# Optimization experiments

Measured on AMD Instinct MI355X. Metric: run time of the kernel, lower is better.

The kernel has to match this reference:

```python
import jax, jax.numpy as jnp
import numpy as np

N = 128  # padded Hadamard size (find_min_power(122))
H1 = W1 = 122

def _hadamard(n):
    H = np.array([[1.0]], dtype=np.float32)
    while H.shape[0] < n:
        H = np.block([[H, H], [H, -H]])
    return H

_H = jnp.asarray(_hadamard(N))  # symmetric 128x128 +/-1 matrix
_DN = ('NCHW', 'OIHW', 'NCHW')

def _conv(x, w, b, stride, pad):
    y = jax.lax.conv_general_dilated(x, w, (stride, stride),
                                     [(pad, pad), (pad, pad)], dimension_numbers=_DN)
    return y + b[None, :, None, None]

def _convT(x, w, b, stride, pad):
    # torch ConvTranspose2d weight layout [in, out, kh, kw]
    k = w.shape[-1]
    wf = jnp.flip(w, (2, 3)).transpose(1, 0, 2, 3)  # -> [out, in, kh, kw]
    p = k - 1 - pad
    y = jax.lax.conv_general_dilated(x, wf, (1, 1), [(p, p), (p, p)],
                                     lhs_dilation=(stride, stride), dimension_numbers=_DN)
    return y + b[None, :, None, None]

def _fwht2(x):
    # fwht along -1 then -2 (dense Hadamard matmul, matching fast=False path)
    x = jnp.einsum('bchw,wk->bchk', x, _H)
    return jnp.einsum('bchw,hk->bckw', x, _H)

def _ifwht2(x):
    x = jnp.einsum('bchw,wk->bchk', x, _H) / N
    return jnp.einsum('bchw,hk->bckw', x, _H) / N

def _pad(x):
    return jnp.pad(x, ((0, 0), (0, 0), (0, N - H1), (0, N - W1)))

def _thresh(x, T):
    aT = jnp.abs(T)
    s = jnp.copysign(jax.nn.relu(jnp.abs(x) - aT), x)
    return s + jnp.sign(s) * aT

def _kl(q):
    e = q.size // 64
    p = jax.nn.sigmoid(jnp.full((64,), 0.001, q.dtype))
    qm = jnp.sum(jax.nn.sigmoid(jnp.abs(q).reshape(e, 64)), axis=0) / e
    return jnp.sum(p * jnp.log(p / qm)) + jnp.sum((1 - p) * jnp.log((1 - p) / (1 - qm)))

def _tv(x, weight):
    b, c, h, w = x.shape
    tv = jnp.abs(x[:, :, 1:, :] - x[:, :, :-1, :]).sum() + \
         jnp.abs(x[:, :, :, 1:] - x[:, :, :, :-1]).sum()
    return weight * tv / (b * c * h * w)

def setup_inputs() -> dict:
    key = jax.random.key(0)
    ks = jax.random.split(key, 16)
    B = 128
    inp = {
        'x': jax.random.normal(ks[0], (B, 1, 256, 256), jnp.float32),
        'val': 0,
        'v1': jax.random.uniform(ks[1], (N, N), jnp.float32),
        'T1': jax.random.uniform(ks[2], (N, N), jnp.float32) / 10,
        'v2': jax.random.uniform(ks[3], (N, N), jnp.float32),
        'T2': jax.random.uniform(ks[4], (N, N), jnp.float32) / 10,
        'v3': jax.random.uniform(ks[5], (N, N), jnp.float32),
        'T3': jax.random.uniform(ks[6], (N, N), jnp.float32) / 10,
        'w1': jax.random.normal(ks[7], (4, 1, 16, 16), jnp.float32) * 0.05,
        'b1': jax.random.normal(ks[8], (4,), jnp.float32) * 0.01,
        'w2': jax.random.normal(ks[9], (4, 4, 7, 7), jnp.float32) * 0.05,
        'b2': jax.random.normal(ks[10], (4,), jnp.float32) * 0.01,
        'w3': jax.random.normal(ks[11], (4, 4, 7, 7), jnp.float32) * 0.05,  # [in,out,kh,kw]
        'b3': jax.random.normal(ks[12], (4,), jnp.float32) * 0.01,
        'w4': jax.random.normal(ks[13], (4, 1, 16, 16), jnp.float32) * 0.05,  # [in,out,kh,kw]
        'b4': jax.random.normal(ks[14], (1,), jnp.float32) * 0.01,
    }
    return inp

def reference(x, val, v1, T1, v2, T2, v3, T3, w1, b1, w2, b2, w3, b3, w4, b4):
    TV_WEIGHT = 0.05  # original draws np.random.uniform(0, 0.1); fixed for determinism
    x1 = _conv(x, w1, b1, 2, 1)                       # [B,4,122,122]
    x6 = _thresh(v1 * _fwht2(_pad(x1)), T1)           # [B,4,128,128]
    x9 = _ifwht2(x6)[..., :H1, :W1]
    x10 = _conv(x9, w2, b2, 1, 3)                     # [B,4,122,122]
    x15 = _thresh(v2 * _fwht2(_pad(x10)), T2)
    x18 = _ifwht2(x15)[..., :H1, :W1]
    x19 = _convT(x18, w3, b3, 1, 3) + x10
    x24 = _thresh(v3 * _fwht2(_pad(x19)), T3)
    x27 = _ifwht2(x24 + x6)[..., :H1, :W1]
    out = _convT(x27, w4, b4, 2, 1) * x               # [B,1,256,256]
    loss = 1.0 * _tv(out, TV_WEIGHT) + 0.1 * (_kl(x6) + _kl(x15) + _kl(x24))
    return out, loss
```

## Files before the change

### kernel.cpp

```cpp
#include <hip/hip_runtime.h>
#include <math.h>

#define PLANE 16384
#define NPLANES 512

__device__ __forceinline__ void fwht2d_reg(float* __restrict__ v, float* __restrict__ xch,
                                           int W, int L) {
#pragma unroll
    for (int m = 1; m <= 2; m <<= 1) {
#pragma unroll
        for (int r = 0; r < 64; ++r) {
            if (!(r & m)) {
                int s = r | m;
                float a = v[r], b = v[s];
                v[r] = a + b; v[s] = a - b;
            }
        }
    }
#pragma unroll
    for (int m = 1; m <= 32; m <<= 1) {
        float sg = (L & m) ? -1.f : 1.f;
#pragma unroll
        for (int r = 0; r < 64; ++r) {
            float p = __shfl_xor(v[r], m);
            v[r] = fmaf(sg, v[r], p);
        }
    }
#pragma unroll
    for (int m = 4; m <= 32; m <<= 1) {
#pragma unroll
        for (int r = 0; r < 64; ++r) {
            if (!(r & m)) {
                int s = r | m;
                float a = v[r], b = v[s];
                v[r] = a + b; v[s] = a - b;
            }
        }
    }
#pragma unroll
    for (int mw = 1; mw <= 2; mw <<= 1) {
        int Wp = W ^ mw;
        float sg = (W & mw) ? -1.f : 1.f;
#pragma unroll
        for (int half = 0; half < 2; ++half) {
            __syncthreads();
#pragma unroll
            for (int j = 0; j < 32; ++j)
                xch[(j * 4 + W) * 64 + L] = v[half * 32 + j];
            __syncthreads();
#pragma unroll
            for (int j = 0; j < 32; ++j) {
                float p = xch[(j * 4 + Wp) * 64 + L];
                v[half * 32 + j] = fmaf(sg, v[half * 32 + j], p);
            }
        }
    }
}

template <bool STORET, bool ADD>
__global__ __launch_bounds__(256) void fwht_kernel_t(
    const float* __restrict__ in, const float* __restrict__ vmat,
    const float* __restrict__ tmat, const float* __restrict__ addbuf,
    float* __restrict__ outThresh, float* __restrict__ outInv,
    float* __restrict__ klpart)
{
    __shared__ float xch[32 * 256];
    const int tid = threadIdx.x;
    const int W = tid >> 6, L = tid & 63;
    const int plane = blockIdx.x;
    const int hbase = W * 32 + ((L >> 5) << 4);
    const int wbase = (L & 31) << 2;
    const float* src = in + (size_t)plane * PLANE;

    float v[64];
#pragma unroll
    for (int g = 0; g < 16; ++g) {
        float4 t = *(const float4*)&src[(hbase + g) * 128 + wbase];
        v[4 * g] = t.x; v[4 * g + 1] = t.y; v[4 * g + 2] = t.z; v[4 * g + 3] = t.w;
    }

    fwht2d_reg(v, xch, W, L);

    float ls0 = 0.f, ls1 = 0.f, ls2 = 0.f, ls3 = 0.f;
#pragma unroll
    for (int g = 0; g < 16; ++g) {
        int rowoff = (hbase + g) * 128 + wbase;
        float4 vm = *(const float4*)&vmat[rowoff];
        float4 tm = *(const float4*)&tmat[rowoff];
        float y0 = v[4 * g]     * vm.x;
        float y1 = v[4 * g + 1] * vm.y;
        float y2 = v[4 * g + 2] * vm.z;
        float y3 = v[4 * g + 3] * vm.w;
        y0 = (fabsf(y0) > fabsf(tm.x)) ? y0 : 0.f;
        y1 = (fabsf(y1) > fabsf(tm.y)) ? y1 : 0.f;
        y2 = (fabsf(y2) > fabsf(tm.z)) ? y2 : 0.f;
        y3 = (fabsf(y3) > fabsf(tm.w)) ? y3 : 0.f;
        ls0 += 1.f / (1.f + __expf(-fabsf(y0)));
        ls1 += 1.f / (1.f + __expf(-fabsf(y1)));
        ls2 += 1.f / (1.f + __expf(-fabsf(y2)));
        ls3 += 1.f / (1.f + __expf(-fabsf(y3)));
        if (STORET) {
            float4 o; o.x = y0; o.y = y1; o.z = y2; o.w = y3;
            *(float4*)&outThresh[(size_t)plane * PLANE + rowoff] = o;
        }
        if (ADD) {
            float4 ad = *(const float4*)&addbuf[(size_t)plane * PLANE + rowoff];
            y0 += ad.x; y1 += ad.y; y2 += ad.z; y3 += ad.w;
        }
        v[4 * g] = y0; v[4 * g + 1] = y1; v[4 * g + 2] = y2; v[4 * g + 3] = y3;
    }
#pragma unroll
    for (int m = 16; m <= 32; m <<= 1) {
        ls0 += __shfl_xor(ls0, m);
        ls1 += __shfl_xor(ls1, m);
        ls2 += __shfl_xor(ls2, m);
        ls3 += __shfl_xor(ls3, m);
    }
    if (L < 16) {
        float4 o; o.x = ls0; o.y = ls1; o.z = ls2; o.w = ls3;
        *(float4*)&klpart[(size_t)(plane * 4 + W) * 64 + 4 * L] = o;
    }

    fwht2d_reg(v, xch, W, L);

    float* dst = outInv + (size_t)plane * PLANE;
    const float s = 1.f / 16384.f;
#pragma unroll
    for (int g = 0; g < 16; ++g) {
        int h = hbase + g;
        bool rv = h < 122;
        float4 o;
        o.x = (rv && wbase + 0 < 122) ? v[4 * g]     * s : 0.f;
        o.y = (rv && wbase + 1 < 122) ? v[4 * g + 1] * s : 0.f;
        o.z = (rv && wbase + 2 < 122) ? v[4 * g + 2] * s : 0.f;
        o.w = (rv && wbase + 3 < 122) ? v[4 * g + 3] * s : 0.f;
        *(float4*)&dst[h * 128 + wbase] = o;
    }
}

__global__ void prep_weights(const float* __restrict__ w3, const float* __restrict__ w4,
                             float* __restrict__ w3c, float* __restrict__ w4p)
{
    int tid = blockIdx.x * 256 + threadIdx.x;
    if (tid < 784) {
        int oc = tid / 196;
        int rem = tid - oc * 196;
        int ic = rem / 49;
        int k = rem - ic * 49;
        int kh = k / 7, kw = k - kh * 7;
        w3c[(oc * 4 + ic) * 49 + k] = w3[(ic * 4 + oc) * 49 + (6 - kh) * 7 + (6 - kw)];
    }
    if (tid < 1024) {
        int u = tid & 7, t = (tid >> 3) & 7, pb = (tid >> 6) & 1, pa = (tid >> 7) & 1, ic = tid >> 8;
        int kh = 2 * t + (pa ? 0 : 1);
        int kw = 2 * u + (pb ? 0 : 1);
        w4p[tid] = w4[ic * 256 + kh * 16 + kw];
    }
}

__global__ __launch_bounds__(256) void conv1_kernel(
    const float* __restrict__ x, const float* __restrict__ w1,
    const float* __restrict__ b1, float* __restrict__ out)
{
    __shared__ float tile[78][80];
    int tx = blockIdx.x, ty = blockIdx.y, b = blockIdx.z;
    int tid = threadIdx.x;
    const float* xp = x + (size_t)b * 65536;
    int r0g = ty * 64 - 1, c0g = tx * 64 - 1;
    for (int i = tid; i < 78 * 78; i += 256) {
        int rr = i / 78, cc = i - rr * 78;
        int gi = r0g + rr, gj = c0g + cc;
        tile[rr][cc] = (gi >= 0 && gi < 256 && gj >= 0 && gj < 256) ? xp[gi * 256 + gj] : 0.f;
    }
    __syncthreads();
    int cg = tid & 7, r = tid >> 3;
    int B = cg * 4;
    float acc[4][4];
#pragma unroll
    for (int oc = 0; oc < 4; ++oc)
#pragma unroll
        for (int c = 0; c < 4; ++c) acc[oc][c] = 0.f;
#pragma unroll 1
    for (int kh = 0; kh < 16; ++kh) {
        float win[24];
        const float* trow = &tile[2 * r + kh][2 * B];
#pragma unroll
        for (int k = 0; k < 6; ++k)
            *(float4*)&win[4 * k] = *(const float4*)&trow[4 * k];
#pragma unroll
        for (int oc = 0; oc < 4; ++oc) {
            const float* wr = w1 + oc * 256 + kh * 16;
#pragma unroll
            for (int kw = 0; kw < 16; ++kw) {
                float wv = wr[kw];
#pragma unroll
                for (int c = 0; c < 4; ++c)
                    acc[oc][c] = fmaf(win[2 * c + kw], wv, acc[oc][c]);
            }
        }
    }
    int oh = ty * 32 + r;
    int owb = tx * 32 + B;
    bool rowv = oh < 122;
#pragma unroll
    for (int oc = 0; oc < 4; ++oc) {
        float bv = b1[oc];
        float4 res;
        res.x = (rowv && owb + 0 < 122) ? acc[oc][0] + bv : 0.f;
        res.y = (rowv && owb + 1 < 122) ? acc[oc][1] + bv : 0.f;
        res.z = (rowv && owb + 2 < 122) ? acc[oc][2] + bv : 0.f;
        res.w = (rowv && owb + 3 < 122) ? acc[oc][3] + bv : 0.f;
        *(float4*)&out[(((size_t)b * 4 + oc) << 14) + (oh << 7) + owb] = res;
    }
}

__global__ __launch_bounds__(256) void conv7_kernel(
    const float* __restrict__ in, const float* __restrict__ w,
    const float* __restrict__ bias, const float* __restrict__ skip,
    float* __restrict__ out)
{
    __shared__ float tile[4][38][40];
    int tx = blockIdx.x, ty = blockIdx.y, b = blockIdx.z;
    int tid = threadIdx.x;
    int r0g = ty * 32 - 3, c0g = tx * 32 - 3;
    for (int i = tid; i < 4 * 38 * 38; i += 256) {
        int ic = i / 1444;
        int rem = i - ic * 1444;
        int rr = rem / 38, cc = rem - rr * 38;
        int gi = r0g + rr, gj = c0g + cc;
        float v = 0.f;
        if (gi >= 0 && gi < 128 && gj >= 0 && gj < 128)
            v = in[(((size_t)b * 4 + ic) << 14) + (gi << 7) + gj];
        tile[ic][rr][cc] = v;
    }
    __syncthreads();
    int cg = tid & 7, r = tid >> 3;
    int B = cg * 4;
    float acc[4][4];
#pragma unroll
    for (int oc = 0; oc < 4; ++oc)
#pragma unroll
        for (int c = 0; c < 4; ++c) acc[oc][c] = 0.f;
#pragma unroll 1
    for (int ic = 0; ic < 4; ++ic) {
#pragma unroll 1
        for (int kh = 0; kh < 7; ++kh) {
            float win[12];
            const float* trow = &tile[ic][r + kh][B];
#pragma unroll
            for (int k = 0; k < 3; ++k)
                *(float4*)&win[4 * k] = *(const float4*)&trow[4 * k];
#pragma unroll
            for (int oc = 0; oc < 4; ++oc) {
                const float* wr = w + (oc * 4 + ic) * 49 + kh * 7;
#pragma unroll
                for (int kw = 0; kw < 7; ++kw) {
                    float wv = wr[kw];
#pragma unroll
                    for (int c = 0; c < 4; ++c)
                        acc[oc][c] = fmaf(win[c + kw], wv, acc[oc][c]);
                }
            }
        }
    }
    int oh = ty * 32 + r;
    int owb = tx * 32 + B;
    bool rowv = oh < 122;
#pragma unroll
    for (int oc = 0; oc < 4; ++oc) {
        size_t o = (((size_t)b * 4 + oc) << 14) + (oh << 7) + owb;
        float4 sv = make_float4(0.f, 0.f, 0.f, 0.f);
        if (skip) sv = *(const float4*)&skip[o];
        float bv = bias[oc];
        float4 res;
        res.x = (rowv && owb + 0 < 122) ? acc[oc][0] + bv + sv.x : 0.f;
        res.y = (rowv && owb + 1 < 122) ? acc[oc][1] + bv + sv.y : 0.f;
        res.z = (rowv && owb + 2 < 122) ? acc[oc][2] + bv + sv.z : 0.f;
        res.w = (rowv && owb + 3 < 122) ? acc[oc][3] + bv + sv.w : 0.f;
        *(float4*)&out[o] = res;
    }
}

#define CT_HALF(T, ROW, PA)                                                    \
    _Pragma("unroll")                                                          \
    for (int pb = 0; pb < 2; ++pb) {                                           \
        const float* w8 = wp + (((ic * 2 + (PA)) * 2 + pb) * 8 + (T)) * 8;     \
        _Pragma("unroll")                                                      \
        for (int u = 0; u < 8; ++u) {                                          \
            float wv = w8[u];                                                  \
            _Pragma("unroll")                                                  \
            for (int c = 0; c < 4; ++c)                                        \
                acc[PA][pb][c] = fmaf(ROW[8 + c + pb - u], wv, acc[PA][pb][c]);\
        }                                                                      \
    }

__global__ __launch_bounds__(256) void convt4_kernel(
    const float* __restrict__ in, const float* __restrict__ wp,
    const float* __restrict__ bias, const float* __restrict__ xin,
    float* __restrict__ out)
{
    __shared__ float tile[4][40][44];
    int tx = blockIdx.x, ty = blockIdx.y, b = blockIdx.z;
    int tid = threadIdx.x;
    int A0 = ty * 32, B0 = tx * 32;
    int r0g = A0 - 7, c0g = B0 - 8;
    for (int i = tid; i < 4 * 40 * 44; i += 256) {
        int ic = i / 1760;
        int rem = i - ic * 1760;
        int rr = rem / 44, cc = rem - rr * 44;
        int gi = r0g + rr, gj = c0g + cc;
        float v = 0.f;
        if (gi >= 0 && gi < 128 && gj >= 0 && gj < 128)
            v = in[(((size_t)b * 4 + ic) << 14) + (gi << 7) + gj];
        tile[ic][rr][cc] = v;
    }
    __syncthreads();
    int cg = tid & 7, ra = tid >> 3;
    float acc[2][2][4];
#pragma unroll
    for (int pa = 0; pa < 2; ++pa)
#pragma unroll
        for (int pb = 0; pb < 2; ++pb)
#pragma unroll
            for (int c = 0; c < 4; ++c) acc[pa][pb][c] = 0.f;
#pragma unroll 1
    for (int ic = 0; ic < 4; ++ic) {
        float bufA[16], bufB[16];
#pragma unroll
        for (int k = 0; k < 4; ++k)
            *(float4*)&bufB[4 * k] = *(const float4*)&tile[ic][ra + 8][4 * cg + 4 * k];
#pragma unroll 1
        for (int t2 = 0; t2 < 8; t2 += 2) {
#pragma unroll
            for (int k = 0; k < 4; ++k)
                *(float4*)&bufA[4 * k] = *(const float4*)&tile[ic][ra + 7 - t2][4 * cg + 4 * k];
            CT_HALF(t2, bufA, 0)
            CT_HALF(t2, bufB, 1)
#pragma unroll
            for (int k = 0; k < 4; ++k)
                *(float4*)&bufB[4 * k] = *(const float4*)&tile[ic][ra + 6 - t2][4 * cg + 4 * k];
            CT_HALF(t2 + 1, bufB, 0)
            CT_HALF(t2 + 1, bufA, 1)
        }
    }
    int oh0 = 2 * (A0 + ra);
    int owb = 2 * (B0 + 4 * cg);
    float bv = bias[0];
#pragma unroll
    for (int pa = 0; pa < 2; ++pa) {
        size_t o = (size_t)b * 65536 + (size_t)(oh0 + pa) * 256 + owb;
        float4 x0 = *(const float4*)&xin[o];
        float4 x1 = *(const float4*)&xin[o + 4];
        float4 r0, r1;
        r0.x = (acc[pa][0][0] + bv) * x0.x;
        r0.y = (acc[pa][1][0] + bv) * x0.y;
        r0.z = (acc[pa][0][1] + bv) * x0.z;
        r0.w = (acc[pa][1][1] + bv) * x0.w;
        r1.x = (acc[pa][0][2] + bv) * x1.x;
        r1.y = (acc[pa][1][2] + bv) * x1.y;
        r1.z = (acc[pa][0][3] + bv) * x1.z;
        r1.w = (acc[pa][1][3] + bv) * x1.w;
        *(float4*)&out[o] = r0;
        *(float4*)&out[o + 4] = r1;
    }
}

__global__ __launch_bounds__(256) void tv_kernel(
    const float* __restrict__ out, float* __restrict__ tvpart)
{
    __shared__ float red[256];
    int tid = threadIdx.x;
    float local = 0.f;
    const int total = 128 * 65536;
    for (int idx = blockIdx.x * 256 + tid; idx < total; idx += gridDim.x * 256) {
        float v = out[idx];
        int hw = idx & 65535;
        if (hw < 65280) local += fabsf(out[idx + 256] - v);
        if ((idx & 255) != 255) local += fabsf(out[idx + 1] - v);
    }
    red[tid] = local;
    __syncthreads();
    for (int s = 128; s > 0; s >>= 1) {
        if (tid < s) red[tid] += red[tid + s];
        __syncthreads();
    }
    if (tid == 0) tvpart[blockIdx.x] = red[0];
}

__global__ __launch_bounds__(256) void reduce1_kernel(
    const float* __restrict__ klpart, const float* __restrict__ tvpart,
    float* __restrict__ klred, float* __restrict__ tvred)
{
    int bid = blockIdx.x;
    int tid = threadIdx.x;
    if (bid < 48) {
        int layer = bid >> 4, chunk = bid & 15;
        int sub = tid >> 6, t = tid & 63;
        const float* base = klpart + (size_t)layer * 131072 + (size_t)chunk * 128 * 64;
        float s = 0.f;
        for (int r = sub; r < 128; r += 4)
            s += base[r * 64 + t];
        __shared__ float red[4][64];
        red[sub][t] = s;
        __syncthreads();
        if (tid < 64)
            klred[(layer * 16 + chunk) * 64 + tid] =
                red[0][tid] + red[1][tid] + red[2][tid] + red[3][tid];
    } else {
        __shared__ float red[256];
        float s = 0.f;
        for (int i = tid; i < 2048; i += 256) s += tvpart[i];
        red[tid] = s;
        __syncthreads();
        for (int st = 128; st > 0; st >>= 1) {
            if (tid < st) red[tid] += red[tid + st];
            __syncthreads();
        }
        if (tid == 0) tvred[0] = red[0];
    }
}

__global__ __launch_bounds__(64) void finalize2_kernel(
    const float* __restrict__ klred, const float* __restrict__ tvred,
    float* __restrict__ lossout)
{
    int t = threadIdx.x;
    float p = 1.f / (1.f + __expf(-0.001f));
    float term = 0.f;
#pragma unroll
    for (int l = 0; l < 3; ++l) {
        float q = 0.f;
#pragma unroll
        for (int c = 0; c < 16; ++c)
            q += klred[(l * 16 + c) * 64 + t];
        float qm = q * (1.f / 131072.f);
        term += p * logf(p / qm) + (1.f - p) * logf((1.f - p) / (1.f - qm));
    }
#pragma unroll
    for (int off = 32; off > 0; off >>= 1)
        term += __shfl_down(term, off);
    if (t == 0)
        lossout[0] = 0.05f * tvred[0] / 8388608.f + 0.1f * term;
}

extern "C" void kernel_launch(void* const* d_in, const int* in_sizes, int n_in,
                              void* d_out, int out_size, void* d_ws, size_t ws_size,
                              hipStream_t stream) {
    (void)in_sizes; (void)n_in; (void)out_size; (void)ws_size;
    const float* x  = (const float*)d_in[0];
    const float* v1 = (const float*)d_in[2];
    const float* T1 = (const float*)d_in[3];
    const float* v2 = (const float*)d_in[4];
    const float* T2 = (const float*)d_in[5];
    const float* v3 = (const float*)d_in[6];
    const float* T3 = (const float*)d_in[7];
    const float* w1 = (const float*)d_in[8];
    const float* b1 = (const float*)d_in[9];
    const float* w2 = (const float*)d_in[10];
    const float* b2 = (const float*)d_in[11];
    const float* w3 = (const float*)d_in[12];
    const float* b3 = (const float*)d_in[13];
    const float* w4 = (const float*)d_in[14];
    const float* b4 = (const float*)d_in[15];
    float* out = (float*)d_out;

    float* W0 = (float*)d_ws;
    float* W1 = W0 + (size_t)NPLANES * PLANE;
    float* W2 = W1 + (size_t)NPLANES * PLANE;
    float* klpart = W2 + (size_t)NPLANES * PLANE;
    float* tvpart = klpart + 3 * 2048 * 64;
    float* klred  = tvpart + 2048;
    float* tvred  = klred + 3072;
    float* w3c = tvred + 64;
    float* w4p = w3c + 784;
    float* x10buf = out;

    prep_weights<<<4, 256, 0, stream>>>(w3, w4, w3c, w4p);
    conv1_kernel<<<dim3(4, 4, 128), 256, 0, stream>>>(x, w1, b1, W0);
    fwht_kernel_t<true, false><<<NPLANES, 256, 0, stream>>>(W0, v1, T1, nullptr, W1, W2, klpart);
    conv7_kernel<<<dim3(4, 4, 128), 256, 0, stream>>>(W2, w2, b2, nullptr, x10buf);
    fwht_kernel_t<false, false><<<NPLANES, 256, 0, stream>>>(x10buf, v2, T2, nullptr, nullptr, W0, klpart + 131072);
    conv7_kernel<<<dim3(4, 4, 128), 256, 0, stream>>>(W0, w3c, b3, x10buf, W2);
    fwht_kernel_t<false, true><<<NPLANES, 256, 0, stream>>>(W2, v3, T3, W1, nullptr, W0, klpart + 2 * 131072);
    convt4_kernel<<<dim3(4, 4, 128), 256, 0, stream>>>(W0, w4p, b4, x, out);
    tv_kernel<<<2048, 256, 0, stream>>>(out, tvpart);
    reduce1_kernel<<<49, 256, 0, stream>>>(klpart, tvpart, klred, tvred);
    finalize2_kernel<<<1, 64, 0, stream>>>(klred, tvred, out + 8388608);
}
```

Before: 375.0 us.

## Register-block two input rows per thread in convT and vectorize TV loss

```diff
diff --git a/kernel.cpp b/kernel.cpp
--- a/kernel.cpp
+++ b/kernel.cpp
@@ -281,7 +281,7 @@
     }
 }
 
-#define CT_HALF(T, ROW, PA)                                                    \
+#define APPLY(P, T, ROW, PA)                                                   \
     _Pragma("unroll")                                                          \
     for (int pb = 0; pb < 2; ++pb) {                                           \
         const float* w8 = wp + (((ic * 2 + (PA)) * 2 + pb) * 8 + (T)) * 8;     \
@@ -290,93 +290,116 @@
             float wv = w8[u];                                                  \
             _Pragma("unroll")                                                  \
             for (int c = 0; c < 4; ++c)                                        \
-                acc[PA][pb][c] = fmaf(ROW[8 + c + pb - u], wv, acc[PA][pb][c]);\
+                acc[P][PA][pb][c] = fmaf(ROW[8 + c + pb - u], wv, acc[P][PA][pb][c]); \
         }                                                                      \
     }
+
+#define LOADROW(BUF, R)                                                        \
+    _Pragma("unroll")                                                          \
+    for (int k = 0; k < 4; ++k)                                                \
+        *(float4*)&BUF[4 * k] = *(const float4*)&tld[(R) * 44 + 4 * cg + 4 * k];
 
 __global__ __launch_bounds__(256) void convt4_kernel(
     const float* __restrict__ in, const float* __restrict__ wp,
     const float* __restrict__ bias, const float* __restrict__ xin,
     float* __restrict__ out)
 {
-    __shared__ float tile[4][40][44];
+    __shared__ float tile[4][72][44];
     int tx = blockIdx.x, ty = blockIdx.y, b = blockIdx.z;
     int tid = threadIdx.x;
-    int A0 = ty * 32, B0 = tx * 32;
+    int A0 = ty * 64, B0 = tx * 32;
     int r0g = A0 - 7, c0g = B0 - 8;
-    for (int i = tid; i < 4 * 40 * 44; i += 256) {
-        int ic = i / 1760;
-        int rem = i - ic * 1760;
+    float* tl = &tile[0][0][0];
+    for (int i = tid; i < 4 * 72 * 44; i += 256) {
+        int ic = i / 3168;
+        int rem = i - ic * 3168;
         int rr = rem / 44, cc = rem - rr * 44;
         int gi = r0g + rr, gj = c0g + cc;
         float v = 0.f;
         if (gi >= 0 && gi < 128 && gj >= 0 && gj < 128)
             v = in[(((size_t)b * 4 + ic) << 14) + (gi << 7) + gj];
-        tile[ic][rr][cc] = v;
+        tl[i] = v;
     }
     __syncthreads();
-    int cg = tid & 7, ra = tid >> 3;
-    float acc[2][2][4];
-#pragma unroll
-    for (int pa = 0; pa < 2; ++pa)
-#pragma unroll
-        for (int pb = 0; pb < 2; ++pb)
-#pragma unroll
-            for (int c = 0; c < 4; ++c) acc[pa][pb][c] = 0.f;
+    int cg = tid & 7, tr = tid >> 3;
+    int rb = 2 * tr;
+    float acc[2][2][2][4];
+#pragma unroll
+    for (int p = 0; p < 2; ++p)
+#pragma unroll
+        for (int pa = 0; pa < 2; ++pa)
+#pragma unroll
+            for (int pb = 0; pb < 2; ++pb)
+#pragma unroll
+                for (int c = 0; c < 4; ++c) acc[p][pa][pb][c] = 0.f;
 #pragma unroll 1
     for (int ic = 0; ic < 4; ++ic) {
-        float bufA[16], bufB[16];
-#pragma unroll
-        for (int k = 0; k < 4; ++k)
-            *(float4*)&bufB[4 * k] = *(const float4*)&tile[ic][ra + 8][4 * cg + 4 * k];
-#pragma unroll 1
-        for (int t2 = 0; t2 < 8; t2 += 2) {
-#pragma unroll
-            for (int k = 0; k < 4; ++k)
-                *(float4*)&bufA[4 * k] = *(const float4*)&tile[ic][ra + 7 - t2][4 * cg + 4 * k];
-            CT_HALF(t2, bufA, 0)
-            CT_HALF(t2, bufB, 1)
-#pragma unroll
-            for (int k = 0; k < 4; ++k)
-                *(float4*)&bufB[4 * k] = *(const float4*)&tile[ic][ra + 6 - t2][4 * cg + 4 * k];
-            CT_HALF(t2 + 1, bufB, 0)
-            CT_HALF(t2 + 1, bufA, 1)
-        }
-    }
-    int oh0 = 2 * (A0 + ra);
+        const float* tld = &tile[ic][0][0];
+        float rA[16], rB[16];
+        LOADROW(rA, rb + 9)
+        LOADROW(rB, rb + 8)
+        APPLY(1, 0, rA, 1)
+        LOADROW(rA, rb + 7)
+        APPLY(0, 0, rB, 1) APPLY(1, 0, rB, 0) APPLY(1, 1, rB, 1)
+        LOADROW(rB, rb + 6)
+        APPLY(0, 0, rA, 0) APPLY(0, 1, rA, 1) APPLY(1, 1, rA, 0) APPLY(1, 2, rA, 1)
+        LOADROW(rA, rb + 5)
+        APPLY(0, 1, rB, 0) APPLY(0, 2, rB, 1) APPLY(1, 2, rB, 0) APPLY(1, 3, rB, 1)
+        LOADROW(rB, rb + 4)
+        APPLY(0, 2, rA, 0) APPLY(0, 3, rA, 1) APPLY(1, 3, rA, 0) APPLY(1, 4, rA, 1)
+        LOADROW(rA, rb + 3)
+        APPLY(0, 3, rB, 0) APPLY(0, 4, rB, 1) APPLY(1, 4, rB, 0) APPLY(1, 5, rB, 1)
+        LOADROW(rB, rb + 2)
+        APPLY(0, 4, rA, 0) APPLY(0, 5, rA, 1) APPLY(1, 5, rA, 0) APPLY(1, 6, rA, 1)
+        LOADROW(rA, rb + 1)
+        APPLY(0, 5, rB, 0) APPLY(0, 6, rB, 1) APPLY(1, 6, rB, 0) APPLY(1, 7, rB, 1)
+        LOADROW(rB, rb + 0)
+        APPLY(0, 6, rA, 0) APPLY(0, 7, rA, 1) APPLY(1, 7, rA, 0)
+        APPLY(0, 7, rB, 0)
+    }
     int owb = 2 * (B0 + 4 * cg);
     float bv = bias[0];
 #pragma unroll
-    for (int pa = 0; pa < 2; ++pa) {
-        size_t o = (size_t)b * 65536 + (size_t)(oh0 + pa) * 256 + owb;
-        float4 x0 = *(const float4*)&xin[o];
-        float4 x1 = *(const float4*)&xin[o + 4];
-        float4 r0, r1;
-        r0.x = (acc[pa][0][0] + bv) * x0.x;
-        r0.y = (acc[pa][1][0] + bv) * x0.y;
-        r0.z = (acc[pa][0][1] + bv) * x0.z;
-        r0.w = (acc[pa][1][1] + bv) * x0.w;
-        r1.x = (acc[pa][0][2] + bv) * x1.x;
-        r1.y = (acc[pa][1][2] + bv) * x1.y;
-        r1.z = (acc[pa][0][3] + bv) * x1.z;
-        r1.w = (acc[pa][1][3] + bv) * x1.w;
-        *(float4*)&out[o] = r0;
-        *(float4*)&out[o + 4] = r1;
+    for (int p = 0; p < 2; ++p) {
+        int ibase = A0 + rb + p;
+#pragma unroll
+        for (int pa = 0; pa < 2; ++pa) {
+            int oh = 2 * ibase + pa;
+            size_t o = (size_t)b * 65536 + (size_t)oh * 256 + owb;
+            float4 x0 = *(const float4*)&xin[o];
+            float4 x1 = *(const float4*)&xin[o + 4];
+            float4 r0, r1;
+            r0.x = (acc[p][pa][0][0] + bv) * x0.x;
+            r0.y = (acc[p][pa][1][0] + bv) * x0.y;
+            r0.z = (acc[p][pa][0][1] + bv) * x0.z;
+            r0.w = (acc[p][pa][1][1] + bv) * x0.w;
+            r1.x = (acc[p][pa][0][2] + bv) * x1.x;
+            r1.y = (acc[p][pa][1][2] + bv) * x1.y;
+            r1.z = (acc[p][pa][0][3] + bv) * x1.z;
+            r1.w = (acc[p][pa][1][3] + bv) * x1.w;
+            *(float4*)&out[o] = r0;
+            *(float4*)&out[o + 4] = r1;
+        }
     }
 }
 
 __global__ __launch_bounds__(256) void tv_kernel(
     const float* __restrict__ out, float* __restrict__ tvpart)
 {
+    const float4* out4 = (const float4*)out;
     __shared__ float red[256];
     int tid = threadIdx.x;
     float local = 0.f;
-    const int total = 128 * 65536;
-    for (int idx = blockIdx.x * 256 + tid; idx < total; idx += gridDim.x * 256) {
-        float v = out[idx];
-        int hw = idx & 65535;
-        if (hw < 65280) local += fabsf(out[idx + 256] - v);
-        if ((idx & 255) != 255) local += fabsf(out[idx + 1] - v);
+    const int total4 = 128 * 65536 / 4;
+    for (int i4 = blockIdx.x * 256 + tid; i4 < total4; i4 += gridDim.x * 256) {
+        float4 a = out4[i4];
+        int i = i4 << 2;
+        local += fabsf(a.y - a.x) + fabsf(a.z - a.y) + fabsf(a.w - a.z);
+        if ((i & 255) != 252) local += fabsf(out[i + 4] - a.w);
+        if ((i & 65535) < 65280) {
+            float4 c = out4[i4 + 64];
+            local += fabsf(c.x - a.x) + fabsf(c.y - a.y) + fabsf(c.z - a.z) + fabsf(c.w - a.w);
+        }
     }
     red[tid] = local;
     __syncthreads();
@@ -482,7 +505,7 @@
     fwht_kernel_t<false, false><<<NPLANES, 256, 0, stream>>>(x10buf, v2, T2, nullptr, nullptr, W0, klpart + 131072);
     conv7_kernel<<<dim3(4, 4, 128), 256, 0, stream>>>(W0, w3c, b3, x10buf, W2);
     fwht_kernel_t<false, true><<<NPLANES, 256, 0, stream>>>(W2, v3, T3, W1, nullptr, W0, klpart + 2 * 131072);
-    convt4_kernel<<<dim3(4, 4, 128), 256, 0, stream>>>(W0, w4p, b4, x, out);
+    convt4_kernel<<<dim3(4, 2, 128), 256, 0, stream>>>(W0, w4p, b4, x, out);
     tv_kernel<<<2048, 256, 0, stream>>>(out, tvpart);
     reduce1_kernel<<<49, 256, 0, stream>>>(klpart, tvpart, klred, tvred);
     finalize2_kernel<<<1, 64, 0, stream>>>(klred, tvred, out + 8388608);
```

New measurement: 389.5 us. 3.8% more time.
